# Kernel optimization log

Measured on AMD Instinct MI355X. Metric: run time of the kernel, lower is better.

## Reference

```python
import jax, jax.numpy as jnp
import numpy as np

def setup_inputs() -> dict:
    key = jax.random.key(0)
    ks = jax.random.split(key, 6)
    ch, cr = 256, 32  # cr = ch // 8
    B, H, W = 4, 64, 64
    sc = 1.0 / np.sqrt(ch)
    return {
        "inputs": jax.random.normal(ks[0], (B, H, W, ch), jnp.float32),
        "Wf": jax.random.normal(ks[1], (ch, cr), jnp.float32) * sc,
        "bf": jnp.zeros((cr,), jnp.float32),
        "Wg": jax.random.normal(ks[2], (ch, cr), jnp.float32) * sc,
        "bg": jnp.zeros((cr,), jnp.float32),
        "Wh": jax.random.normal(ks[3], (ch, cr), jnp.float32) * sc,
        "bh": jnp.zeros((cr,), jnp.float32),
        "Wv": jax.random.normal(ks[4], (cr, ch), jnp.float32) * (1.0 / np.sqrt(cr)),
        "bv": jnp.zeros((ch,), jnp.float32),
        "gamma": jnp.zeros((1,), jnp.float32),
    }

def reference(inputs, Wf, bf, Wg, bg, Wh, bh, Wv, bv, gamma):
    B, H, W, C = inputs.shape
    x = inputs.reshape(B, H * W, C)  # [B, N, C]
    f = x @ Wf + bf  # [B, N, cr] (keys)
    g = x @ Wg + bg  # [B, N, cr] (queries)
    h = x @ Wh + bh  # [B, N, cr] (values)
    s = jnp.einsum('bnk,bmk->bnm', g, f)  # [B, N, N]
    beta = jax.nn.softmax(s, axis=-1)
    v = jnp.einsum('bnm,bmk->bnk', beta, h)  # [B, N, cr]
    o = v @ Wv + bv  # [B, N, C]
    out = gamma * o + x
    return out.reshape(B, H, W, C)
```

## Files before the change

kernel.cpp:

```cpp
#include <hip/hip_runtime.h>

#define B_SZ  4
#define N_TOK 4096
#define CH    256
#define CR    32
#define SEG   512
#define KT    64
#define NITER (SEG / KT)
#define LOG2E 1.44269504f
#define SHIFT2 (12.0f * 1.44269504f)

typedef __attribute__((ext_vector_type(8))) short bf16x8;
typedef __attribute__((ext_vector_type(4))) float f32x4;

__device__ inline ushort f2bf(float x) {
    uint u = __float_as_uint(x);
    u += 0x7fff + ((u >> 16) & 1);
    return (ushort)(u >> 16);
}
__device__ inline uint pk2bf(float a, float b) {
    return __builtin_amdgcn_perm(__float_as_uint(b), __float_as_uint(a), 0x07060302);
}

__global__ __launch_bounds__(256) void prep_kernel(
    const float* __restrict__ Wf, const float* __restrict__ Wg,
    const float* __restrict__ Wh, const float* __restrict__ Wv,
    ushort* __restrict__ wft, ushort* __restrict__ wgt,
    ushort* __restrict__ wht, ushort* __restrict__ wvt)
{
    int t = threadIdx.x, blk = blockIdx.x;
    if (blk < 3) {
        const float* W  = (blk == 0) ? Wf : (blk == 1) ? Wg : Wh;
        ushort*      Wt = (blk == 0) ? wft : (blk == 1) ? wgt : wht;
        int j = t & 31, half = t >> 5;
        ushort tmp[32];
        #pragma unroll
        for (int kk = 0; kk < 32; ++kk)
            tmp[kk] = f2bf(W[(half * 32 + kk) * CR + j]);
        ushort* dst = Wt + (size_t)j * CH + half * 32;
        #pragma unroll
        for (int k8 = 0; k8 < 4; ++k8)
            *(bf16x8*)(dst + k8 * 8) = *(bf16x8*)&tmp[k8 * 8];
    } else {
        ushort tmp[32];
        #pragma unroll
        for (int k = 0; k < CR; ++k) tmp[k] = f2bf(Wv[k * CH + t]);
        ushort* dst = wvt + (size_t)t * CR;
        #pragma unroll
        for (int k8 = 0; k8 < 4; ++k8)
            *(bf16x8*)(dst + k8 * 8) = *(bf16x8*)&tmp[k8 * 8];
    }
}

__global__ __launch_bounds__(256) void proj_kernel(
    const float* __restrict__ x,
    const ushort* __restrict__ wft, const ushort* __restrict__ wgt, const ushort* __restrict__ wht,
    const float* __restrict__ bf_, const float* __restrict__ bg, const float* __restrict__ bh,
    ushort* __restrict__ fo, ushort* __restrict__ go, ushort* __restrict__ hto)
{
    __shared__ f32x4 accx[3][6][64];
    int t  = threadIdx.x;
    int wv = t >> 6, L = t & 63, nl = L & 15, Q = L >> 4;
    int row_t = blockIdx.x * 16;
    int b = row_t >> 12, tok0 = row_t & 4095;

    const float* xrow = x + (size_t)(row_t + nl) * CH;
    f32x4 A[6];
    #pragma unroll
    for (int i = 0; i < 6; ++i) A[i] = (f32x4){0.f, 0.f, 0.f, 0.f};

    #pragma unroll
    for (int c2 = 0; c2 < 2; ++c2) {
        int off = wv * 64 + c2 * 32 + Q * 8;
        float4 lo = *(const float4*)(xrow + off);
        float4 hi = *(const float4*)(xrow + off + 4);
        bf16x8 xa;
        xa[0] = (short)f2bf(lo.x); xa[1] = (short)f2bf(lo.y);
        xa[2] = (short)f2bf(lo.z); xa[3] = (short)f2bf(lo.w);
        xa[4] = (short)f2bf(hi.x); xa[5] = (short)f2bf(hi.y);
        xa[6] = (short)f2bf(hi.z); xa[7] = (short)f2bf(hi.w);

        bf16x8 wf0 = *(const bf16x8*)(wft + (size_t)nl * CH + off);
        bf16x8 wf1 = *(const bf16x8*)(wft + (size_t)(16 + nl) * CH + off);
        bf16x8 wg0 = *(const bf16x8*)(wgt + (size_t)nl * CH + off);
        bf16x8 wg1 = *(const bf16x8*)(wgt + (size_t)(16 + nl) * CH + off);
        bf16x8 wh0 = *(const bf16x8*)(wht + (size_t)nl * CH + off);
        bf16x8 wh1 = *(const bf16x8*)(wht + (size_t)(16 + nl) * CH + off);

        A[0] = __builtin_amdgcn_mfma_f32_16x16x32_bf16(xa, wf0, A[0], 0, 0, 0);
        A[1] = __builtin_amdgcn_mfma_f32_16x16x32_bf16(xa, wf1, A[1], 0, 0, 0);
        A[2] = __builtin_amdgcn_mfma_f32_16x16x32_bf16(xa, wg0, A[2], 0, 0, 0);
        A[3] = __builtin_amdgcn_mfma_f32_16x16x32_bf16(xa, wg1, A[3], 0, 0, 0);
        A[4] = __builtin_amdgcn_mfma_f32_16x16x32_bf16(wh0, xa, A[4], 0, 0, 0);
        A[5] = __builtin_amdgcn_mfma_f32_16x16x32_bf16(wh1, xa, A[5], 0, 0, 0);
    }

    if (wv > 0) {
        #pragma unroll
        for (int i = 0; i < 6; ++i) accx[wv - 1][i][L] = A[i];
    }
    __syncthreads();
    if (wv == 0) {
        #pragma unroll
        for (int i = 0; i < 6; ++i) {
            f32x4 s0 = accx[0][i][L], s1 = accx[1][i][L], s2 = accx[2][i][L];
            A[i] = A[i] + s0 + s1 + s2;
        }
        float bF0 = bf_[nl], bF1 = bf_[16 + nl];
        float bG0 = bg[nl] * LOG2E, bG1 = bg[16 + nl] * LOG2E;
        #pragma unroll
        for (int r = 0; r < 4; ++r) {
            size_t ro = (size_t)(row_t + Q * 4 + r) * CR;
            fo[ro + nl]      = f2bf(A[0][r] + bF0);
            fo[ro + 16 + nl] = f2bf(A[1][r] + bF1);
            go[ro + nl]      = f2bf(fmaf(A[2][r], LOG2E, bG0));
            go[ro + 16 + nl] = f2bf(fmaf(A[3][r], LOG2E, bG1));
        }
        ushort* hb = hto + (size_t)b * CR * N_TOK + tok0 + nl;
        #pragma unroll
        for (int r = 0; r < 4; ++r) {
            int ch = Q * 4 + r;
            hb[(size_t)ch * N_TOK]        = f2bf(A[4][r] + bh[ch]);
            hb[(size_t)(16 + ch) * N_TOK] = f2bf(A[5][r] + bh[16 + ch]);
        }
    }
}

__global__ __launch_bounds__(512, 4) void attn_kernel(
    const ushort* __restrict__ f, const ushort* __restrict__ g,
    const ushort* __restrict__ ht, const ushort* __restrict__ wvt,
    const float* __restrict__ bv, const float* __restrict__ gamma,
    const float* __restrict__ x, float* __restrict__ out)
{
    __shared__ unsigned long long smem_raw[38912 / 8];
    ushort (*pls)[32][76]  = (ushort (*)[32][76])smem_raw;
    float  (*obuf)[32][33] = (float (*)[32][33])smem_raw;
    float  (*lbuf)[32]     = (float (*)[32])((char*)smem_raw + 33792);
    ushort (*oc)[48]       = (ushort (*)[48])((char*)smem_raw + 34816);

    int t  = threadIdx.x;
    int wv = t >> 6;
    int L  = t & 63;
    int nl = L & 15;
    int Q  = L >> 4;
    int b  = blockIdx.x >> 7;
    int q0 = (blockIdx.x & 127) * 32;

    const ushort* fb  = f  + (size_t)b * N_TOK * CR;
    const ushort* htb = ht + (size_t)b * CR * N_TOK;

    bf16x8 gB0 = *(const bf16x8*)(g + ((size_t)b * N_TOK + q0 + nl) * CR + Q * 8);
    bf16x8 gB1 = *(const bf16x8*)(g + ((size_t)b * N_TOK + q0 + 16 + nl) * CR + Q * 8);

    f32x4 acc00 = {0,0,0,0}, acc01 = {0,0,0,0};
    f32x4 acc10 = {0,0,0,0}, acc11 = {0,0,0,0};
    const f32x4 zf = {0,0,0,0};
    float lsum0 = 0.f, lsum1 = 0.f;

    int k0 = wv * SEG;
    bf16x8 Ac0 = *(const bf16x8*)(fb + (size_t)(k0 +  0 + nl) * CR + Q * 8);
    bf16x8 Ac1 = *(const bf16x8*)(fb + (size_t)(k0 + 16 + nl) * CR + Q * 8);
    bf16x8 Ac2 = *(const bf16x8*)(fb + (size_t)(k0 + 32 + nl) * CR + Q * 8);
    bf16x8 Ac3 = *(const bf16x8*)(fb + (size_t)(k0 + 48 + nl) * CR + Q * 8);
    const ushort* h0 = htb + (size_t)nl * N_TOK + k0;
    bf16x8 Bc0 = *(const bf16x8*)(h0 + Q * 8);
    bf16x8 Bc1 = *(const bf16x8*)(h0 + (size_t)16 * N_TOK + Q * 8);
    bf16x8 Bc2 = *(const bf16x8*)(h0 + 32 + Q * 8);
    bf16x8 Bc3 = *(const bf16x8*)(h0 + (size_t)16 * N_TOK + 32 + Q * 8);

    #pragma unroll 2
    for (int it = 0; it < NITER; ++it) {
        int kn = wv * SEG + ((it + 1) & (NITER - 1)) * KT;
        const ushort* fn = fb + (size_t)kn * CR;
        bf16x8 An0 = *(const bf16x8*)(fn + (size_t)( 0 + nl) * CR + Q * 8);
        bf16x8 An1 = *(const bf16x8*)(fn + (size_t)(16 + nl) * CR + Q * 8);
        bf16x8 An2 = *(const bf16x8*)(fn + (size_t)(32 + nl) * CR + Q * 8);
        bf16x8 An3 = *(const bf16x8*)(fn + (size_t)(48 + nl) * CR + Q * 8);
        const ushort* hn = htb + (size_t)nl * N_TOK + kn;
        bf16x8 Bn0 = *(const bf16x8*)(hn + Q * 8);
        bf16x8 Bn1 = *(const bf16x8*)(hn + (size_t)16 * N_TOK + Q * 8);
        bf16x8 Bn2 = *(const bf16x8*)(hn + 32 + Q * 8);
        bf16x8 Bn3 = *(const bf16x8*)(hn + (size_t)16 * N_TOK + 32 + Q * 8);

        #pragma unroll
        for (int sk = 0; sk < 4; ++sk) {
            bf16x8 Ak = (sk == 0) ? Ac0 : (sk == 1) ? Ac1 : (sk == 2) ? Ac2 : Ac3;
            f32x4 s0 = __builtin_amdgcn_mfma_f32_16x16x32_bf16(Ak, gB0, zf, 0, 0, 0);
            f32x4 s1 = __builtin_amdgcn_mfma_f32_16x16x32_bf16(Ak, gB1, zf, 0, 0, 0);
            float p0 = exp2f(s0[0] - SHIFT2), p1 = exp2f(s0[1] - SHIFT2);
            float p2 = exp2f(s0[2] - SHIFT2), p3 = exp2f(s0[3] - SHIFT2);
            lsum0 += (p0 + p1) + (p2 + p3);
            uint2 w; w.x = pk2bf(p0, p1); w.y = pk2bf(p2, p3);
            *(uint2*)&pls[wv][nl][sk * 16 + Q * 4] = w;
            p0 = exp2f(s1[0] - SHIFT2); p1 = exp2f(s1[1] - SHIFT2);
            p2 = exp2f(s1[2] - SHIFT2); p3 = exp2f(s1[3] - SHIFT2);
            lsum1 += (p0 + p1) + (p2 + p3);
            w.x = pk2bf(p0, p1); w.y = pk2bf(p2, p3);
            *(uint2*)&pls[wv][16 + nl][sk * 16 + Q * 4] = w;
        }

        bf16x8 aP00 = *(const bf16x8*)&pls[wv][     nl][ 0 + Q * 8];
        bf16x8 aP01 = *(const bf16x8*)&pls[wv][     nl][32 + Q * 8];
        bf16x8 aP10 = *(const bf16x8*)&pls[wv][16 + nl][ 0 + Q * 8];
        bf16x8 aP11 = *(const bf16x8*)&pls[wv][16 + nl][32 + Q * 8];

        acc00 = __builtin_amdgcn_mfma_f32_16x16x32_bf16(aP00, Bc0, acc00, 0, 0, 0);
        acc01 = __builtin_amdgcn_mfma_f32_16x16x32_bf16(aP00, Bc1, acc01, 0, 0, 0);
        acc10 = __builtin_amdgcn_mfma_f32_16x16x32_bf16(aP10, Bc0, acc10, 0, 0, 0);
        acc11 = __builtin_amdgcn_mfma_f32_16x16x32_bf16(aP10, Bc1, acc11, 0, 0, 0);
        acc00 = __builtin_amdgcn_mfma_f32_16x16x32_bf16(aP01, Bc2, acc00, 0, 0, 0);
        acc01 = __builtin_amdgcn_mfma_f32_16x16x32_bf16(aP01, Bc3, acc01, 0, 0, 0);
        acc10 = __builtin_amdgcn_mfma_f32_16x16x32_bf16(aP11, Bc2, acc10, 0, 0, 0);
        acc11 = __builtin_amdgcn_mfma_f32_16x16x32_bf16(aP11, Bc3, acc11, 0, 0, 0);

        Ac0 = An0; Ac1 = An1; Ac2 = An2; Ac3 = An3;
        Bc0 = Bn0; Bc1 = Bn1; Bc2 = Bn2; Bc3 = Bn3;
    }

    lsum0 += __shfl_xor(lsum0, 16); lsum0 += __shfl_xor(lsum0, 32);
    lsum1 += __shfl_xor(lsum1, 16); lsum1 += __shfl_xor(lsum1, 32);

    __syncthreads();
    #pragma unroll
    for (int r = 0; r < 4; ++r) {
        obuf[wv][     Q * 4 + r][nl]      = acc00[r];
        obuf[wv][     Q * 4 + r][16 + nl] = acc01[r];
        obuf[wv][16 + Q * 4 + r][nl]      = acc10[r];
        obuf[wv][16 + Q * 4 + r][16 + nl] = acc11[r];
    }
    if (L < 16) { lbuf[wv][nl] = lsum0; lbuf[wv][16 + nl] = lsum1; }
    __syncthreads();

    {
        int ch = t & 31, qb = t >> 5;
        #pragma unroll
        for (int qq = qb; qq < 32; qq += 16) {
            float s = 0.f, Lq = 0.f;
            #pragma unroll
            for (int w = 0; w < 8; ++w) { s += obuf[w][qq][ch]; Lq += lbuf[w][qq]; }
            oc[qq][ch] = f2bf(s / Lq);
        }
    }
    __syncthreads();

    bf16x8 aO0 = *(const bf16x8*)&oc[     nl][Q * 8];
    bf16x8 aO1 = *(const bf16x8*)&oc[16 + nl][Q * 8];
    float gm = gamma[0];
    const float* xb = x   + ((size_t)b * N_TOK + q0) * CH;
    float*       ob = out + ((size_t)b * N_TOK + q0) * CH;
    #pragma unroll
    for (int i = 0; i < 2; ++i) {
        int nb = wv * 2 + i;
        bf16x8 bW = *(const bf16x8*)(wvt + (size_t)(nb * 16 + nl) * CR + Q * 8);
        f32x4 d0 = __builtin_amdgcn_mfma_f32_16x16x32_bf16(aO0, bW, zf, 0, 0, 0);
        f32x4 d1 = __builtin_amdgcn_mfma_f32_16x16x32_bf16(aO1, bW, zf, 0, 0, 0);
        int c = nb * 16 + nl;
        float bvc = bv[c];
        #pragma unroll
        for (int r = 0; r < 4; ++r) {
            int qa = Q * 4 + r;
            ob[qa * CH + c]        = fmaf(gm, d0[r] + bvc, xb[qa * CH + c]);
            ob[(16 + qa) * CH + c] = fmaf(gm, d1[r] + bvc, xb[(16 + qa) * CH + c]);
        }
    }
}

extern "C" void kernel_launch(void* const* d_in, const int* in_sizes, int n_in,
                              void* d_out, int out_size, void* d_ws, size_t ws_size,
                              hipStream_t stream) {
    const float* x     = (const float*)d_in[0];
    const float* Wf    = (const float*)d_in[1];
    const float* bf_   = (const float*)d_in[2];
    const float* Wg    = (const float*)d_in[3];
    const float* bg    = (const float*)d_in[4];
    const float* Wh    = (const float*)d_in[5];
    const float* bh    = (const float*)d_in[6];
    const float* Wv    = (const float*)d_in[7];
    const float* bv    = (const float*)d_in[8];
    const float* gamma = (const float*)d_in[9];
    float* out = (float*)d_out;

    const size_t T = (size_t)B_SZ * N_TOK * CR;
    ushort* fo  = (ushort*)d_ws;
    ushort* go  = fo + T;
    ushort* hto = go + T;
    ushort* wvt = hto + T;
    ushort* wft = wvt + CH * CR;
    ushort* wgt = wft + CH * CR;
    ushort* wht = wgt + CH * CR;

    prep_kernel<<<4, 256, 0, stream>>>(Wf, Wg, Wh, Wv, wft, wgt, wht, wvt);
    proj_kernel<<<B_SZ * N_TOK / 16, 256, 0, stream>>>(x, wft, wgt, wht, bf_, bg, bh, fo, go, hto);
    attn_kernel<<<B_SZ * (N_TOK / 32), 512, 0, stream>>>(fo, go, hto, wvt, bv, gamma, x, out);
}
```

Measured before the change: 125.6 us.

## Software-pipeline attention loop with double-buffered P tiles and prefetch residual x

Halves the key tile to 32 and restructures the attention loop so each iteration computes QK^T and exp for the current tile while running the PV MFMAs on the previous tile's probabilities. The probabilities sit in a double-buffered LDS region. The residual x, bias and gamma loads move before the reduction so their latency overlaps the LDS reduction and syncs. The risk is more loop iterations with less work in each, plus extra register pressure from the prefetched x values at 4 blocks per SM.

New measurement: 196.2 us. 56.2% more time.

```diff
diff --git a/kernel.cpp b/kernel.cpp
--- a/kernel.cpp
+++ b/kernel.cpp
@@ -5,7 +5,7 @@
 #define CH    256
 #define CR    32
 #define SEG   512
-#define KT    64
+#define KT    32
 #define NITER (SEG / KT)
 #define LOG2E 1.44269504f
 #define SHIFT2 (12.0f * 1.44269504f)
@@ -132,11 +132,11 @@
     const float* __restrict__ bv, const float* __restrict__ gamma,
     const float* __restrict__ x, float* __restrict__ out)
 {
-    __shared__ unsigned long long smem_raw[38912 / 8];
-    ushort (*pls)[32][76]  = (ushort (*)[32][76])smem_raw;
-    float  (*obuf)[32][33] = (float (*)[32][33])smem_raw;
-    float  (*lbuf)[32]     = (float (*)[32])((char*)smem_raw + 33792);
-    ushort (*oc)[48]       = (ushort (*)[48])((char*)smem_raw + 34816);
+    __shared__ unsigned long long smem_raw[37888 / 8];
+    ushort (*pls)[8][32][36] = (ushort (*)[8][32][36])smem_raw;
+    float  (*obuf)[32][33]   = (float (*)[32][33])smem_raw;
+    float  (*lbuf)[32]       = (float (*)[32])((char*)smem_raw + 33792);
+    ushort (*oc)[48]         = (ushort (*)[48])((char*)smem_raw + 34816);
 
     int t  = threadIdx.x;
     int wv = t >> 6;
@@ -158,64 +158,94 @@
     float lsum0 = 0.f, lsum1 = 0.f;
 
     int k0 = wv * SEG;
-    bf16x8 Ac0 = *(const bf16x8*)(fb + (size_t)(k0 +  0 + nl) * CR + Q * 8);
+    bf16x8 Ac0 = *(const bf16x8*)(fb + (size_t)(k0 +      nl) * CR + Q * 8);
     bf16x8 Ac1 = *(const bf16x8*)(fb + (size_t)(k0 + 16 + nl) * CR + Q * 8);
-    bf16x8 Ac2 = *(const bf16x8*)(fb + (size_t)(k0 + 32 + nl) * CR + Q * 8);
-    bf16x8 Ac3 = *(const bf16x8*)(fb + (size_t)(k0 + 48 + nl) * CR + Q * 8);
-    const ushort* h0 = htb + (size_t)nl * N_TOK + k0;
-    bf16x8 Bc0 = *(const bf16x8*)(h0 + Q * 8);
-    bf16x8 Bc1 = *(const bf16x8*)(h0 + (size_t)16 * N_TOK + Q * 8);
-    bf16x8 Bc2 = *(const bf16x8*)(h0 + 32 + Q * 8);
-    bf16x8 Bc3 = *(const bf16x8*)(h0 + (size_t)16 * N_TOK + 32 + Q * 8);
+    bf16x8 Bc0 = *(const bf16x8*)(htb + (size_t)nl * N_TOK + k0 + Q * 8);
+    bf16x8 Bc1 = *(const bf16x8*)(htb + (size_t)(16 + nl) * N_TOK + k0 + Q * 8);
+    bf16x8 An0 = *(const bf16x8*)(fb + (size_t)(k0 + KT +      nl) * CR + Q * 8);
+    bf16x8 An1 = *(const bf16x8*)(fb + (size_t)(k0 + KT + 16 + nl) * CR + Q * 8);
+    bf16x8 Bn0 = *(const bf16x8*)(htb + (size_t)nl * N_TOK + k0 + KT + Q * 8);
+    bf16x8 Bn1 = *(const bf16x8*)(htb + (size_t)(16 + nl) * N_TOK + k0 + KT + Q * 8);
+
+    {
+        f32x4 s0 = __builtin_amdgcn_mfma_f32_16x16x32_bf16(Ac0, gB0, zf, 0, 0, 0);
+        f32x4 s1 = __builtin_amdgcn_mfma_f32_16x16x32_bf16(Ac1, gB0, zf, 0, 0, 0);
+        f32x4 s2 = __builtin_amdgcn_mfma_f32_16x16x32_bf16(Ac0, gB1, zf, 0, 0, 0);
+        f32x4 s3 = __builtin_amdgcn_mfma_f32_16x16x32_bf16(Ac1, gB1, zf, 0, 0, 0);
+        float p0, p1, p2, p3; uint2 w;
+        p0=exp2f(s0[0]-SHIFT2); p1=exp2f(s0[1]-SHIFT2); p2=exp2f(s0[2]-SHIFT2); p3=exp2f(s0[3]-SHIFT2);
+        lsum0 += (p0+p1)+(p2+p3); w.x=pk2bf(p0,p1); w.y=pk2bf(p2,p3);
+        *(uint2*)&pls[0][wv][nl][Q * 4] = w;
+        p0=exp2f(s1[0]-SHIFT2); p1=exp2f(s1[1]-SHIFT2); p2=exp2f(s1[2]-SHIFT2); p3=exp2f(s1[3]-SHIFT2);
+        lsum0 += (p0+p1)+(p2+p3); w.x=pk2bf(p0,p1); w.y=pk2bf(p2,p3);
+        *(uint2*)&pls[0][wv][nl][16 + Q * 4] = w;
+        p0=exp2f(s2[0]-SHIFT2); p1=exp2f(s2[1]-SHIFT2); p2=exp2f(s2[2]-SHIFT2); p3=exp2f(s2[3]-SHIFT2);
+        lsum1 += (p0+p1)+(p2+p3); w.x=pk2bf(p0,p1); w.y=pk2bf(p2,p3);
+        *(uint2*)&pls[0][wv][16 + nl][Q * 4] = w;
+        p0=exp2f(s3[0]-SHIFT2); p1=exp2f(s3[1]-SHIFT2); p2=exp2f(s3[2]-SHIFT2); p3=exp2f(s3[3]-SHIFT2);
+        lsum1 += (p0+p1)+(p2+p3); w.x=pk2bf(p0,p1); w.y=pk2bf(p2,p3);
+        *(uint2*)&pls[0][wv][16 + nl][16 + Q * 4] = w;
+    }
+    bf16x8 Bp0 = Bc0, Bp1 = Bc1;
+    Ac0 = An0; Ac1 = An1; Bc0 = Bn0; Bc1 = Bn1;
 
     #pragma unroll 2
-    for (int it = 0; it < NITER; ++it) {
-        int kn = wv * SEG + ((it + 1) & (NITER - 1)) * KT;
-        const ushort* fn = fb + (size_t)kn * CR;
-        bf16x8 An0 = *(const bf16x8*)(fn + (size_t)( 0 + nl) * CR + Q * 8);
-        bf16x8 An1 = *(const bf16x8*)(fn + (size_t)(16 + nl) * CR + Q * 8);
-        bf16x8 An2 = *(const bf16x8*)(fn + (size_t)(32 + nl) * CR + Q * 8);
-        bf16x8 An3 = *(const bf16x8*)(fn + (size_t)(48 + nl) * CR + Q * 8);
-        const ushort* hn = htb + (size_t)nl * N_TOK + kn;
-        bf16x8 Bn0 = *(const bf16x8*)(hn + Q * 8);
-        bf16x8 Bn1 = *(const bf16x8*)(hn + (size_t)16 * N_TOK + Q * 8);
-        bf16x8 Bn2 = *(const bf16x8*)(hn + 32 + Q * 8);
-        bf16x8 Bn3 = *(const bf16x8*)(hn + (size_t)16 * N_TOK + 32 + Q * 8);
-
-        #pragma unroll
-        for (int sk = 0; sk < 4; ++sk) {
-            bf16x8 Ak = (sk == 0) ? Ac0 : (sk == 1) ? Ac1 : (sk == 2) ? Ac2 : Ac3;
-            f32x4 s0 = __builtin_amdgcn_mfma_f32_16x16x32_bf16(Ak, gB0, zf, 0, 0, 0);
-            f32x4 s1 = __builtin_amdgcn_mfma_f32_16x16x32_bf16(Ak, gB1, zf, 0, 0, 0);
-            float p0 = exp2f(s0[0] - SHIFT2), p1 = exp2f(s0[1] - SHIFT2);
-            float p2 = exp2f(s0[2] - SHIFT2), p3 = exp2f(s0[3] - SHIFT2);
-            lsum0 += (p0 + p1) + (p2 + p3);
-            uint2 w; w.x = pk2bf(p0, p1); w.y = pk2bf(p2, p3);
-            *(uint2*)&pls[wv][nl][sk * 16 + Q * 4] = w;
-            p0 = exp2f(s1[0] - SHIFT2); p1 = exp2f(s1[1] - SHIFT2);
-            p2 = exp2f(s1[2] - SHIFT2); p3 = exp2f(s1[3] - SHIFT2);
-            lsum1 += (p0 + p1) + (p2 + p3);
-            w.x = pk2bf(p0, p1); w.y = pk2bf(p2, p3);
-            *(uint2*)&pls[wv][16 + nl][sk * 16 + Q * 4] = w;
-        }
-
-        bf16x8 aP00 = *(const bf16x8*)&pls[wv][     nl][ 0 + Q * 8];
-        bf16x8 aP01 = *(const bf16x8*)&pls[wv][     nl][32 + Q * 8];
-        bf16x8 aP10 = *(const bf16x8*)&pls[wv][16 + nl][ 0 + Q * 8];
-        bf16x8 aP11 = *(const bf16x8*)&pls[wv][16 + nl][32 + Q * 8];
-
-        acc00 = __builtin_amdgcn_mfma_f32_16x16x32_bf16(aP00, Bc0, acc00, 0, 0, 0);
-        acc01 = __builtin_amdgcn_mfma_f32_16x16x32_bf16(aP00, Bc1, acc01, 0, 0, 0);
-        acc10 = __builtin_amdgcn_mfma_f32_16x16x32_bf16(aP10, Bc0, acc10, 0, 0, 0);
-        acc11 = __builtin_amdgcn_mfma_f32_16x16x32_bf16(aP10, Bc1, acc11, 0, 0, 0);
-        acc00 = __builtin_amdgcn_mfma_f32_16x16x32_bf16(aP01, Bc2, acc00, 0, 0, 0);
-        acc01 = __builtin_amdgcn_mfma_f32_16x16x32_bf16(aP01, Bc3, acc01, 0, 0, 0);
-        acc10 = __builtin_amdgcn_mfma_f32_16x16x32_bf16(aP11, Bc2, acc10, 0, 0, 0);
-        acc11 = __builtin_amdgcn_mfma_f32_16x16x32_bf16(aP11, Bc3, acc11, 0, 0, 0);
-
-        Ac0 = An0; Ac1 = An1; Ac2 = An2; Ac3 = An3;
-        Bc0 = Bn0; Bc1 = Bn1; Bc2 = Bn2; Bc3 = Bn3;
-    }
+    for (int it = 1; it < NITER; ++it) {
+        int pb = (it - 1) & 1, cb = it & 1;
+        bf16x8 aP0 = *(const bf16x8*)&pls[pb][wv][     nl][Q * 8];
+        bf16x8 aP1 = *(const bf16x8*)&pls[pb][wv][16 + nl][Q * 8];
+        int kn = k0 + ((it + 1 < NITER) ? it + 1 : 0) * KT;
+        An0 = *(const bf16x8*)(fb + (size_t)(kn +      nl) * CR + Q * 8);
+        An1 = *(const bf16x8*)(fb + (size_t)(kn + 16 + nl) * CR + Q * 8);
+        Bn0 = *(const bf16x8*)(htb + (size_t)nl * N_TOK + kn + Q * 8);
+        Bn1 = *(const bf16x8*)(htb + (size_t)(16 + nl) * N_TOK + kn + Q * 8);
+        f32x4 s0 = __builtin_amdgcn_mfma_f32_16x16x32_bf16(Ac0, gB0, zf, 0, 0, 0);
+        f32x4 s1 = __builtin_amdgcn_mfma_f32_16x16x32_bf16(Ac1, gB0, zf, 0, 0, 0);
+        f32x4 s2 = __builtin_amdgcn_mfma_f32_16x16x32_bf16(Ac0, gB1, zf, 0, 0, 0);
+        f32x4 s3 = __builtin_amdgcn_mfma_f32_16x16x32_bf16(Ac1, gB1, zf, 0, 0, 0);
+        float p0, p1, p2, p3; uint2 w;
+        p0=exp2f(s0[0]-SHIFT2); p1=exp2f(s0[1]-SHIFT2); p2=exp2f(s0[2]-SHIFT2); p3=exp2f(s0[3]-SHIFT2);
+        lsum0 += (p0+p1)+(p2+p3); w.x=pk2bf(p0,p1); w.y=pk2bf(p2,p3);
+        *(uint2*)&pls[cb][wv][nl][Q * 4] = w;
+        p0=exp2f(s1[0]-SHIFT2); p1=exp2f(s1[1]-SHIFT2); p2=exp2f(s1[2]-SHIFT2); p3=exp2f(s1[3]-SHIFT2);
+        lsum0 += (p0+p1)+(p2+p3); w.x=pk2bf(p0,p1); w.y=pk2bf(p2,p3);
+        *(uint2*)&pls[cb][wv][nl][16 + Q * 4] = w;
+        p0=exp2f(s2[0]-SHIFT2); p1=exp2f(s2[1]-SHIFT2); p2=exp2f(s2[2]-SHIFT2); p3=exp2f(s2[3]-SHIFT2);
+        lsum1 += (p0+p1)+(p2+p3); w.x=pk2bf(p0,p1); w.y=pk2bf(p2,p3);
+        *(uint2*)&pls[cb][wv][16 + nl][Q * 4] = w;
+        p0=exp2f(s3[0]-SHIFT2); p1=exp2f(s3[1]-SHIFT2); p2=exp2f(s3[2]-SHIFT2); p3=exp2f(s3[3]-SHIFT2);
+        lsum1 += (p0+p1)+(p2+p3); w.x=pk2bf(p0,p1); w.y=pk2bf(p2,p3);
+        *(uint2*)&pls[cb][wv][16 + nl][16 + Q * 4] = w;
+        acc00 = __builtin_amdgcn_mfma_f32_16x16x32_bf16(aP0, Bp0, acc00, 0, 0, 0);
+        acc01 = __builtin_amdgcn_mfma_f32_16x16x32_bf16(aP0, Bp1, acc01, 0, 0, 0);
+        acc10 = __builtin_amdgcn_mfma_f32_16x16x32_bf16(aP1, Bp0, acc10, 0, 0, 0);
+        acc11 = __builtin_amdgcn_mfma_f32_16x16x32_bf16(aP1, Bp1, acc11, 0, 0, 0);
+        Bp0 = Bc0; Bp1 = Bc1;
+        Ac0 = An0; Ac1 = An1; Bc0 = Bn0; Bc1 = Bn1;
+    }
+    {
+        int pb = (NITER - 1) & 1;
+        bf16x8 aP0 = *(const bf16x8*)&pls[pb][wv][     nl][Q * 8];
+        bf16x8 aP1 = *(const bf16x8*)&pls[pb][wv][16 + nl][Q * 8];
+        acc00 = __builtin_amdgcn_mfma_f32_16x16x32_bf16(aP0, Bp0, acc00, 0, 0, 0);
+        acc01 = __builtin_amdgcn_mfma_f32_16x16x32_bf16(aP0, Bp1, acc01, 0, 0, 0);
+        acc10 = __builtin_amdgcn_mfma_f32_16x16x32_bf16(aP1, Bp0, acc10, 0, 0, 0);
+        acc11 = __builtin_amdgcn_mfma_f32_16x16x32_bf16(aP1, Bp1, acc11, 0, 0, 0);
+    }
+
+    const float* xb = x + ((size_t)b * N_TOK + q0) * CH;
+    int c0 = (wv * 2 + 0) * 16 + nl;
+    int c1 = (wv * 2 + 1) * 16 + nl;
+    float xr0[8], xr1[8];
+    #pragma unroll
+    for (int r = 0; r < 4; ++r) {
+        xr0[r]     = xb[(Q * 4 + r) * CH + c0];
+        xr0[4 + r] = xb[(16 + Q * 4 + r) * CH + c0];
+        xr1[r]     = xb[(Q * 4 + r) * CH + c1];
+        xr1[4 + r] = xb[(16 + Q * 4 + r) * CH + c1];
+    }
+    float gm = gamma[0];
+    float bv0 = bv[c0], bv1 = bv[c1];
 
     lsum0 += __shfl_xor(lsum0, 16); lsum0 += __shfl_xor(lsum0, 32);
     lsum1 += __shfl_xor(lsum1, 16); lsum1 += __shfl_xor(lsum1, 32);
@@ -245,22 +275,21 @@
 
     bf16x8 aO0 = *(const bf16x8*)&oc[     nl][Q * 8];
     bf16x8 aO1 = *(const bf16x8*)&oc[16 + nl][Q * 8];
-    float gm = gamma[0];
-    const float* xb = x   + ((size_t)b * N_TOK + q0) * CH;
     float*       ob = out + ((size_t)b * N_TOK + q0) * CH;
-    #pragma unroll
-    for (int i = 0; i < 2; ++i) {
-        int nb = wv * 2 + i;
-        bf16x8 bW = *(const bf16x8*)(wvt + (size_t)(nb * 16 + nl) * CR + Q * 8);
-        f32x4 d0 = __builtin_amdgcn_mfma_f32_16x16x32_bf16(aO0, bW, zf, 0, 0, 0);
-        f32x4 d1 = __builtin_amdgcn_mfma_f32_16x16x32_bf16(aO1, bW, zf, 0, 0, 0);
-        int c = nb * 16 + nl;
-        float bvc = bv[c];
+    {
+        bf16x8 bW0 = *(const bf16x8*)(wvt + (size_t)c0 * CR + Q * 8);
+        bf16x8 bW1 = *(const bf16x8*)(wvt + (size_t)c1 * CR + Q * 8);
+        f32x4 d00 = __builtin_amdgcn_mfma_f32_16x16x32_bf16(aO0, bW0, zf, 0, 0, 0);
+        f32x4 d10 = __builtin_amdgcn_mfma_f32_16x16x32_bf16(aO1, bW0, zf, 0, 0, 0);
+        f32x4 d01 = __builtin_amdgcn_mfma_f32_16x16x32_bf16(aO0, bW1, zf, 0, 0, 0);
+        f32x4 d11 = __builtin_amdgcn_mfma_f32_16x16x32_bf16(aO1, bW1, zf, 0, 0, 0);
         #pragma unroll
         for (int r = 0; r < 4; ++r) {
             int qa = Q * 4 + r;
-            ob[qa * CH + c]        = fmaf(gm, d0[r] + bvc, xb[qa * CH + c]);
-            ob[(16 + qa) * CH + c] = fmaf(gm, d1[r] + bvc, xb[(16 + qa) * CH + c]);
+            ob[qa * CH + c0]        = fmaf(gm, d00[r] + bv0, xr0[r]);
+            ob[(16 + qa) * CH + c0] = fmaf(gm, d10[r] + bv0, xr0[4 + r]);
+            ob[qa * CH + c1]        = fmaf(gm, d01[r] + bv1, xr1[r]);
+            ob[(16 + qa) * CH + c1] = fmaf(gm, d11[r] + bv1, xr1[4 + r]);
         }
     }
 }
```
